# Kernel tuning notes

Hardware: AMD Instinct MI355X
Metric: run time of the kernel (lower is better)

Reference implementation:

```python
import jax, jax.numpy as jnp
import numpy as np

H = 16  # attention heads


def setup_inputs() -> dict:
    key = jax.random.key(0)
    k0, k1, k2 = jax.random.split(key, 3)
    B, T, C = 2, 2048, 1024
    x = jax.random.normal(k0, (B, T, C), dtype=jnp.float32)
    W_attn = jax.random.normal(k1, (3 * C, C), dtype=jnp.float32) * 0.02
    W_proj = jax.random.normal(k2, (C, C), dtype=jnp.float32) * 0.02
    b_proj = jnp.zeros((C,), dtype=jnp.float32)
    return {"x": x, "W_attn": W_attn, "W_proj": W_proj, "b_proj": b_proj}


def reference(x, W_attn, W_proj, b_proj):
    # Eval-mode (dropout = identity), rotational_embeddings=False, flash=False path.
    B, T, C = x.shape
    d = C // H
    qkv = jnp.einsum('btc,fc->btf', x, W_attn)          # [B,T,3C] fused QKV proj
    q, k, v = jnp.split(qkv, 3, axis=-1)
    # [B,T,C] -> [B,H,T,d]
    q = q.reshape(B, T, H, d).transpose(0, 2, 1, 3)
    k = k.reshape(B, T, H, d).transpose(0, 2, 1, 3)
    v = v.reshape(B, T, H, d).transpose(0, 2, 1, 3)
    scale = 1.0 / np.sqrt(d).astype(np.float32)
    att = jnp.einsum('bhqd,bhkd->bhqk', q, k) * scale    # full TxT scores (no mask)
    att = jax.nn.softmax(att, axis=-1)
    y = jnp.einsum('bhqk,bhkd->bhqd', att, v)            # [B,H,T,d]
    y = y.transpose(0, 2, 1, 3).reshape(B, T, C)
    return jnp.einsum('btc,oc->bto', y, W_proj) + b_proj
```

## Files before the change

### kernel.cpp

```cpp
#include <hip/hip_runtime.h>
#include <hip/hip_bf16.h>
#include <stdint.h>

typedef __attribute__((ext_vector_type(8))) short bf16x8;
typedef __attribute__((ext_vector_type(4))) float f32x4;
typedef __attribute__((ext_vector_type(4))) unsigned u32x4;

#define MFMA16(A,B,C) __builtin_amdgcn_mfma_f32_16x16x32_bf16(A,B,C,0,0,0)


__device__ inline void gld_lds16(const __hip_bfloat16* g, __hip_bfloat16* l) {
  __builtin_amdgcn_global_load_lds(
      (const __attribute__((address_space(1))) void*)g,
      (__attribute__((address_space(3))) void*)l, 16, 0, 0);
}

__device__ inline unsigned pkbf(float a, float b) {
  __hip_bfloat162 t = __float22bfloat162_rn(float2{a, b});
  return *(unsigned*)&t;
}

__device__ inline void quad_mix(unsigned &a, unsigned &b) {
#if __has_builtin(__builtin_amdgcn_permlane32_swap) && __has_builtin(__builtin_amdgcn_permlane16_swap)
  auto r1 = __builtin_amdgcn_permlane32_swap(a, b, false, false);
  auto r2 = __builtin_amdgcn_permlane16_swap(r1[0], r1[1], false, false);
  a = r2[0];
  b = r2[1];
#else
  int lane = (int)(threadIdx.x & 63);
  int g = lane >> 4;
  int lm = lane & 15;
  int slo = (((g << 1) & 3) << 4) | lm;
  int shi = ((((g << 1) | 1) & 3) << 4) | lm;
  unsigned t0 = (unsigned)__shfl((int)a, slo, 64);
  unsigned t1 = (unsigned)__shfl((int)b, slo, 64);
  unsigned t2 = (unsigned)__shfl((int)a, shi, 64);
  unsigned t3 = (unsigned)__shfl((int)b, shi, 64);
  bool hi = g >= 2;
  unsigned na = hi ? t1 : t0;
  unsigned nb = hi ? t3 : t2;
  a = na;
  b = nb;
#endif
}

__global__ __launch_bounds__(256)
void cvt_bf16(const float* __restrict__ s0, __hip_bfloat16* __restrict__ d0, int n0,
              const float* __restrict__ s1, __hip_bfloat16* __restrict__ d1, int n1,
              const float* __restrict__ s2, __hip_bfloat16* __restrict__ d2, int n2)
{
  const float* s; __hip_bfloat16* d; int n;
  if      (blockIdx.y == 0) { s = s0; d = d0; n = n0; }
  else if (blockIdx.y == 1) { s = s1; d = d1; n = n1; }
  else                      { s = s2; d = d2; n = n2; }
  int idx = (blockIdx.x * 256 + threadIdx.x) * 8;
  if (idx >= n) return;
  float4 u0 = *(const float4*)(s + idx);
  float4 u1 = *(const float4*)(s + idx + 4);
  __hip_bfloat16 t[8];
  t[0] = __float2bfloat16(u0.x); t[1] = __float2bfloat16(u0.y);
  t[2] = __float2bfloat16(u0.z); t[3] = __float2bfloat16(u0.w);
  t[4] = __float2bfloat16(u1.x); t[5] = __float2bfloat16(u1.y);
  t[6] = __float2bfloat16(u1.z); t[7] = __float2bfloat16(u1.w);
  *(int4*)(d + idx) = *(const int4*)t;
}

template<int BM, int BN, typename TC>
__global__ __launch_bounds__(256)
void gemm_bt(const __hip_bfloat16* __restrict__ A,
             const __hip_bfloat16* __restrict__ B,
             TC* __restrict__ C,
             const float* __restrict__ bias,
             __hip_bfloat16* __restrict__ vtg,
             int M, int N, int K)
{
  constexpr int MI = BM / 32;
  constexpr int NJ = BN / 32;
  constexpr int NP = (BM + BN) / 64;

  __shared__ __align__(16) __hip_bfloat16 As[BM * 32];
  __shared__ __align__(16) __hip_bfloat16 Bs[BN * 32];

  const int tid  = threadIdx.x;
  const int lane = tid & 63;
  const int w    = tid >> 6;
  const int lm   = lane & 15;
  const int g    = lane >> 4;

  const int bm = blockIdx.y * BM;
  const int bn = blockIdx.x * BN;
  const int rm = (w >> 1) * (BM / 2);
  const int cn = (w & 1) * (BN / 2);

  const f32x4 fzero = {0.0f, 0.0f, 0.0f, 0.0f};
  f32x4 acc[MI][NJ];
  for (int i = 0; i < MI; i++)
    for (int j = 0; j < NJ; j++)
      acc[i][j] = fzero;

  for (int k0 = 0; k0 < K; k0 += 32) {
    __syncthreads();
#pragma unroll
    for (int p = 0; p < NP; p++) {
      int c = tid + p * 256;
      if (c < BM * 4)
        gld_lds16(&A[(size_t)(bm + (c >> 2)) * K + k0 + (c & 3) * 8], &As[c * 8]);
      else {
        int cb = c - BM * 4;
        gld_lds16(&B[(size_t)(bn + (cb >> 2)) * K + k0 + (cb & 3) * 8], &Bs[cb * 8]);
      }
    }
    __syncthreads();

    bf16x8 af[MI], bfr[NJ];
#pragma unroll
    for (int i = 0; i < MI; i++)
      af[i] = *(const bf16x8*)&As[(rm + 16 * i + lm) * 32 + 8 * g];
#pragma unroll
    for (int j = 0; j < NJ; j++)
      bfr[j] = *(const bf16x8*)&Bs[(cn + 16 * j + lm) * 32 + 8 * g];
#pragma unroll
    for (int i = 0; i < MI; i++)
#pragma unroll
      for (int j = 0; j < NJ; j++)
        acc[i][j] = MFMA16(af[i], bfr[j], acc[i][j]);
  }

  if (vtg != nullptr && bn >= 2048) {
#pragma unroll
    for (int j = 0; j < NJ; j++) {
      int colv = bn + cn + 16 * j + lm - 2048;
      int vh = colv >> 6, dd = colv & 63;
#pragma unroll
      for (int i = 0; i < MI; i++) {
        int m0 = bm + rm + 16 * i + 4 * g;
        int bb = m0 >> 11, t0 = m0 & 2047;
        __hip_bfloat16 t4[4];
#pragma unroll
        for (int r = 0; r < 4; r++) t4[r] = __float2bfloat16(acc[i][j][r]);
        *(int2*)&vtg[((size_t)(bb * 16 + vh) * 64 + dd) * 2048 + t0] =
            *(const int2*)t4;
      }
    }
    return;
  }

  const float qs = (vtg != nullptr && bn < 1024) ? (0.125f * 1.4426950408889634f)
                                                 : 1.0f;
#pragma unroll
  for (int j = 0; j < NJ; j++) {
    int coln = bn + cn + 16 * j + lm;
    float bv = bias ? bias[coln] : 0.0f;
#pragma unroll
    for (int i = 0; i < MI; i++) {
#pragma unroll
      for (int r = 0; r < 4; r++) {
        int rowm = bm + rm + 16 * i + 4 * g + r;
        float v = acc[i][j][r] * qs + bv;
        if constexpr (sizeof(TC) == 2)
          C[(size_t)rowm * N + coln] = __float2bfloat16(v);
        else
          C[(size_t)rowm * N + coln] = v;
      }
    }
  }
}

__global__ __launch_bounds__(256)
void mha(const __hip_bfloat16* __restrict__ qkv,
         const __hip_bfloat16* __restrict__ vtg,
         __hip_bfloat16* __restrict__ yout,
         __hip_bfloat16* __restrict__ po,
         float* __restrict__ pl,
         int nsteps)
{
  const int T = 2048, F = 3072, Cc = 1024;
  const int bh = blockIdx.x;
  const int b  = bh >> 4, h = bh & 15;
  const int qb0 = blockIdx.y * 128;
  const int z   = blockIdx.z;
  const int kvb = z * 32 * nsteps;

  const int tid  = threadIdx.x;
  const int lane = tid & 63;
  const int w    = tid >> 6;
  const int lm   = lane & 15;
  const int g    = lane >> 4;

  __shared__ __align__(16) __hip_bfloat16 Ks[2][32 * 64];
  __shared__ __align__(16) __hip_bfloat16 Vs[2][64 * 32];

  const size_t rowbase = (size_t)b * T * F;
  const int hoff = h * 64;
  const __hip_bfloat16* Kbase = qkv + rowbase + 1024 + hoff;
  const __hip_bfloat16* Vtb   = vtg + (size_t)(b * 16 + h) * 64 * 2048;

  const int qw = qb0 + 32 * w;
  bf16x8 aq[2][2];
#pragma unroll
  for (int mt = 0; mt < 2; mt++)
#pragma unroll
    for (int e = 0; e < 2; e++)
      aq[mt][e] = *(const bf16x8*)
          &qkv[rowbase + (size_t)(qw + 16 * mt + lm) * F + hoff + 32 * e + 8 * g];

  const f32x4 fzero = {0.0f, 0.0f, 0.0f, 0.0f};
  f32x4 yacc[2][4];
  float lsum[2] = {0.0f, 0.0f};
#pragma unroll
  for (int mt = 0; mt < 2; mt++)
#pragma unroll
    for (int c = 0; c < 4; c++) yacc[mt][c] = fzero;

  const int r0  = tid >> 3;
  const int swK = (tid & 7) ^ (r0 & 7);
  const int vdd = tid >> 2;
  const int vk  = (tid & 3) ^ ((tid >> 3) & 3);
  const int sxK = lm & 7;
  const int sxV = (lm >> 1) & 3;

  gld_lds16(Kbase + (size_t)(kvb + r0) * F + swK * 8, &Ks[0][tid * 8]);
  gld_lds16(Vtb + (size_t)vdd * 2048 + kvb + vk * 8, &Vs[0][tid * 8]);

  for (int t = 0; t < nsteps; t++) {
    const int buf = t & 1;
    __syncthreads();
    if (t + 1 < nsteps) {
      const int kvn = kvb + (t + 1) * 32;
      gld_lds16(Kbase + (size_t)(kvn + r0) * F + swK * 8, &Ks[buf ^ 1][tid * 8]);
      gld_lds16(Vtb + (size_t)vdd * 2048 + kvn + vk * 8, &Vs[buf ^ 1][tid * 8]);
    }

    bf16x8 kf[2][2];
#pragma unroll
    for (int c2 = 0; c2 < 2; c2++) {
      kf[c2][0] = *(const bf16x8*)&Ks[buf][(16 * c2 + lm) * 64 + ((0 + g) ^ sxK) * 8];
      kf[c2][1] = *(const bf16x8*)&Ks[buf][(16 * c2 + lm) * 64 + ((4 + g) ^ sxK) * 8];
    }
#pragma unroll
    for (int mt = 0; mt < 2; mt++) {
      f32x4 st[2];
#pragma unroll
      for (int c2 = 0; c2 < 2; c2++) {
        st[c2] = MFMA16(kf[c2][0], aq[mt][0], fzero);
        st[c2] = MFMA16(kf[c2][1], aq[mt][1], st[c2]);
      }

      unsigned pkv[2][2];
#pragma unroll
      for (int c2 = 0; c2 < 2; c2++)
#pragma unroll
        for (int u = 0; u < 2; u++) {
          float p0 = __builtin_amdgcn_exp2f(st[c2][2 * u]);
          float p1 = __builtin_amdgcn_exp2f(st[c2][2 * u + 1]);
          lsum[mt] += p0 + p1;
          pkv[c2][u] = pkbf(p0, p1);
        }

      unsigned f0 = pkv[0][0], f2 = pkv[1][0];
      quad_mix(f0, f2);
      unsigned f1 = pkv[0][1], f3 = pkv[1][1];
      quad_mix(f1, f3);
      u32x4 fv = {f0, f1, f2, f3};
      bf16x8 ap = __builtin_bit_cast(bf16x8, fv);

#pragma unroll
      for (int c = 0; c < 4; c++) {
        bf16x8 bv = *(const bf16x8*)&Vs[buf][(16 * c + lm) * 32 + (g ^ sxV) * 8];
        yacc[mt][c] = MFMA16(ap, bv, yacc[mt][c]);
      }
    }
  }

  float lred[2];
#pragma unroll
  for (int mt = 0; mt < 2; mt++) {
    float ls = lsum[mt];
    ls += __shfl_xor(ls, 16);
    ls += __shfl_xor(ls, 32);
    lred[mt] = ls;
  }

#pragma unroll
  for (int mt = 0; mt < 2; mt++) {
    if (yout != nullptr) {
      float rv[4];
#pragma unroll
      for (int r = 0; r < 4; r++)
        rv[r] = 1.0f / __shfl(lred[mt], 4 * g + r, 64);
#pragma unroll
      for (int c = 0; c < 4; c++)
#pragma unroll
        for (int r = 0; r < 4; r++) {
          int qrow = qw + 16 * mt + 4 * g + r;
          yout[(size_t)(b * T + qrow) * Cc + hoff + 16 * c + lm] =
              __float2bfloat16(yacc[mt][c][r] * rv[r]);
        }
    } else {
      __hip_bfloat16* pz = po + (size_t)z * 4096 * 1024;
      float* plz = pl + (size_t)z * 4096 * 16;
#pragma unroll
      for (int c = 0; c < 4; c++)
#pragma unroll
        for (int r = 0; r < 4; r++) {
          int qrow = qw + 16 * mt + 4 * g + r;
          pz[(size_t)(b * T + qrow) * Cc + hoff + 16 * c + lm] =
              __float2bfloat16(yacc[mt][c][r]);
        }
      if (lane < 16)
        plz[(b * T + qw + 16 * mt + lane) * 16 + h] = lred[mt];
    }
  }
}

__global__ __launch_bounds__(256)
void combine(const __hip_bfloat16* __restrict__ po,
             const float* __restrict__ pl,
             __hip_bfloat16* __restrict__ y)
{
  int idx = (blockIdx.x * 256 + threadIdx.x) * 8;
  int row = idx >> 10, c = idx & 1023, h = c >> 6;
  float la = pl[row * 16 + h];
  float lb = pl[4096 * 16 + row * 16 + h];
  float rinv = 1.0f / (la + lb);
  const __hip_bfloat16* pa = po + idx;
  const __hip_bfloat16* pb = po + 4096 * 1024 + idx;
  __hip_bfloat16 t[8];
#pragma unroll
  for (int j = 0; j < 8; j++)
    t[j] = __float2bfloat16(
        (__bfloat162float(pa[j]) + __bfloat162float(pb[j])) * rinv);
  *(int4*)(y + idx) = *(const int4*)t;
}

extern "C" void kernel_launch(void* const* d_in, const int* in_sizes, int n_in,
                              void* d_out, int out_size, void* d_ws, size_t ws_size,
                              hipStream_t stream)
{
  const float* x  = (const float*)d_in[0];
  const float* Wa = (const float*)d_in[1];
  const float* Wp = (const float*)d_in[2];
  const float* bp = (const float*)d_in[3];
  float* out = (float*)d_out;

  const int BT = 4096, C = 1024, F3 = 3072;
  char* ws = (char*)d_ws;
  __hip_bfloat16* qkv  = (__hip_bfloat16*)ws;
  __hip_bfloat16* vtg  = (__hip_bfloat16*)(ws + 25165824);
  __hip_bfloat16* xbf  = (__hip_bfloat16*)(ws + 33554432);
  __hip_bfloat16* yb   = xbf;
  __hip_bfloat16* Wabf = (__hip_bfloat16*)(ws + 41943040);
  __hip_bfloat16* Wpbf = (__hip_bfloat16*)(ws + 48234496);
  __hip_bfloat16* Opar = (__hip_bfloat16*)(ws + 50331648);
  float*          lpar = (float*)(ws + 67108864);
  const size_t need_split = 67633152;

  cvt_bf16<<<dim3(2048, 3), 256, 0, stream>>>(
      x, xbf, BT * C, Wa, Wabf, F3 * C, Wp, Wpbf, C * C);
  gemm_bt<128, 128, __hip_bfloat16>
      <<<dim3(F3 / 128, BT / 128), 256, 0, stream>>>(xbf, Wabf, qkv, nullptr, vtg,
                                                     BT, F3, C);
  if (ws_size >= need_split) {
    mha<<<dim3(32, 16, 2), 256, 0, stream>>>(qkv, vtg, nullptr, Opar, lpar, 32);
    combine<<<dim3(BT * C / 2048), 256, 0, stream>>>(Opar, lpar, yb);
  } else {
    mha<<<dim3(32, 16, 1), 256, 0, stream>>>(qkv, vtg, yb, nullptr, nullptr, 64);
  }
  gemm_bt<64, 128, float>
      <<<dim3(C / 128, BT / 64), 256, 0, stream>>>(yb, Wpbf, out, bp, nullptr,
                                                   BT, C, C);
}
```

Before: 206.6 us.

## Fuse fp32-to-bf16 conversion and split-KV combine into GEMM tile loads

Removes the separate conversion kernel and the combine kernel. The QKV GEMM now reads fp32 x and W_attn directly and converts them to bf16 while staging into LDS. The output GEMM merges the two split-KV partials and normalizes them while loading its A tile, and its tile grows to 128x128. This saves two launches and the bf16 intermediate round trips to memory, but the GEMM loads become synchronous register loads instead of async global-to-LDS copies, and the weights are reconverted by every block that reads them. The non-split fallback path is also dropped.

```diff
diff --git a/kernel.cpp b/kernel.cpp
--- a/kernel.cpp
+++ b/kernel.cpp
@@ -13,6 +13,37 @@
   __builtin_amdgcn_global_load_lds(
       (const __attribute__((address_space(1))) void*)g,
       (__attribute__((address_space(3))) void*)l, 16, 0, 0);
+}
+
+__device__ inline void cvt_store8(const float* __restrict__ g,
+                                  __hip_bfloat16* __restrict__ l) {
+  float4 u0 = *(const float4*)g;
+  float4 u1 = *(const float4*)(g + 4);
+  __hip_bfloat162 t[4];
+  t[0] = __float22bfloat162_rn(float2{u0.x, u0.y});
+  t[1] = __float22bfloat162_rn(float2{u0.z, u0.w});
+  t[2] = __float22bfloat162_rn(float2{u1.x, u1.y});
+  t[3] = __float22bfloat162_rn(float2{u1.z, u1.w});
+  *(int4*)l = *(const int4*)t;
+}
+
+__device__ inline void comb_store8(const __hip_bfloat16* __restrict__ a,
+                                   const __hip_bfloat16* __restrict__ b,
+                                   float rinv,
+                                   __hip_bfloat16* __restrict__ l) {
+  int4 av = *(const int4*)a;
+  int4 bv = *(const int4*)b;
+  const __hip_bfloat162* ap = (const __hip_bfloat162*)&av;
+  const __hip_bfloat162* bp = (const __hip_bfloat162*)&bv;
+  __hip_bfloat162 t[4];
+#pragma unroll
+  for (int i = 0; i < 4; i++) {
+    float2 fa = __bfloat1622float2(ap[i]);
+    float2 fb = __bfloat1622float2(bp[i]);
+    t[i] = __float22bfloat162_rn(float2{(fa.x + fb.x) * rinv,
+                                        (fa.y + fb.y) * rinv});
+  }
+  *(int4*)l = *(const int4*)t;
 }
 
 __device__ inline unsigned pkbf(float a, float b) {
@@ -45,41 +76,14 @@
 }
 
 __global__ __launch_bounds__(256)
-void cvt_bf16(const float* __restrict__ s0, __hip_bfloat16* __restrict__ d0, int n0,
-              const float* __restrict__ s1, __hip_bfloat16* __restrict__ d1, int n1,
-              const float* __restrict__ s2, __hip_bfloat16* __restrict__ d2, int n2)
+void gemm_qkv(const float* __restrict__ A,
+              const float* __restrict__ B,
+              __hip_bfloat16* __restrict__ C,
+              __hip_bfloat16* __restrict__ vtg,
+              int M, int N, int K)
 {
-  const float* s; __hip_bfloat16* d; int n;
-  if      (blockIdx.y == 0) { s = s0; d = d0; n = n0; }
-  else if (blockIdx.y == 1) { s = s1; d = d1; n = n1; }
-  else                      { s = s2; d = d2; n = n2; }
-  int idx = (blockIdx.x * 256 + threadIdx.x) * 8;
-  if (idx >= n) return;
-  float4 u0 = *(const float4*)(s + idx);
-  float4 u1 = *(const float4*)(s + idx + 4);
-  __hip_bfloat16 t[8];
-  t[0] = __float2bfloat16(u0.x); t[1] = __float2bfloat16(u0.y);
-  t[2] = __float2bfloat16(u0.z); t[3] = __float2bfloat16(u0.w);
-  t[4] = __float2bfloat16(u1.x); t[5] = __float2bfloat16(u1.y);
-  t[6] = __float2bfloat16(u1.z); t[7] = __float2bfloat16(u1.w);
-  *(int4*)(d + idx) = *(const int4*)t;
-}
-
-template<int BM, int BN, typename TC>
-__global__ __launch_bounds__(256)
-void gemm_bt(const __hip_bfloat16* __restrict__ A,
-             const __hip_bfloat16* __restrict__ B,
-             TC* __restrict__ C,
-             const float* __restrict__ bias,
-             __hip_bfloat16* __restrict__ vtg,
-             int M, int N, int K)
-{
-  constexpr int MI = BM / 32;
-  constexpr int NJ = BN / 32;
-  constexpr int NP = (BM + BN) / 64;
-
-  __shared__ __align__(16) __hip_bfloat16 As[BM * 32];
-  __shared__ __align__(16) __hip_bfloat16 Bs[BN * 32];
+  __shared__ __align__(16) __hip_bfloat16 As[128 * 32];
+  __shared__ __align__(16) __hip_bfloat16 Bs[128 * 32];
 
   const int tid  = threadIdx.x;
   const int lane = tid & 63;
@@ -87,52 +91,51 @@
   const int lm   = lane & 15;
   const int g    = lane >> 4;
 
-  const int bm = blockIdx.y * BM;
-  const int bn = blockIdx.x * BN;
-  const int rm = (w >> 1) * (BM / 2);
-  const int cn = (w & 1) * (BN / 2);
+  const int bm = blockIdx.y * 128;
+  const int bn = blockIdx.x * 128;
+  const int rm = (w >> 1) * 64;
+  const int cn = (w & 1) * 64;
+
+  const int row0 = tid >> 2;
+  const int kc   = (tid & 3) * 8;
 
   const f32x4 fzero = {0.0f, 0.0f, 0.0f, 0.0f};
-  f32x4 acc[MI][NJ];
-  for (int i = 0; i < MI; i++)
-    for (int j = 0; j < NJ; j++)
+  f32x4 acc[4][4];
+  for (int i = 0; i < 4; i++)
+    for (int j = 0; j < 4; j++)
       acc[i][j] = fzero;
 
   for (int k0 = 0; k0 < K; k0 += 32) {
     __syncthreads();
 #pragma unroll
-    for (int p = 0; p < NP; p++) {
-      int c = tid + p * 256;
-      if (c < BM * 4)
-        gld_lds16(&A[(size_t)(bm + (c >> 2)) * K + k0 + (c & 3) * 8], &As[c * 8]);
-      else {
-        int cb = c - BM * 4;
-        gld_lds16(&B[(size_t)(bn + (cb >> 2)) * K + k0 + (cb & 3) * 8], &Bs[cb * 8]);
-      }
-    }
-    __syncthreads();
-
-    bf16x8 af[MI], bfr[NJ];
-#pragma unroll
-    for (int i = 0; i < MI; i++)
+    for (int p = 0; p < 2; p++) {
+      int row = row0 + 64 * p;
+      cvt_store8(A + (size_t)(bm + row) * K + k0 + kc, &As[row * 32 + kc]);
+      cvt_store8(B + (size_t)(bn + row) * K + k0 + kc, &Bs[row * 32 + kc]);
+    }
+    __syncthreads();
+
+    bf16x8 af[4], bfr[4];
+#pragma unroll
+    for (int i = 0; i < 4; i++)
       af[i] = *(const bf16x8*)&As[(rm + 16 * i + lm) * 32 + 8 * g];
 #pragma unroll
-    for (int j = 0; j < NJ; j++)
+    for (int j = 0; j < 4; j++)
       bfr[j] = *(const bf16x8*)&Bs[(cn + 16 * j + lm) * 32 + 8 * g];
 #pragma unroll
-    for (int i = 0; i < MI; i++)
-#pragma unroll
-      for (int j = 0; j < NJ; j++)
+    for (int i = 0; i < 4; i++)
+#pragma unroll
+      for (int j = 0; j < 4; j++)
         acc[i][j] = MFMA16(af[i], bfr[j], acc[i][j]);
   }
 
-  if (vtg != nullptr && bn >= 2048) {
-#pragma unroll
-    for (int j = 0; j < NJ; j++) {
+  if (bn >= 2048) {
+#pragma unroll
+    for (int j = 0; j < 4; j++) {
       int colv = bn + cn + 16 * j + lm - 2048;
       int vh = colv >> 6, dd = colv & 63;
 #pragma unroll
-      for (int i = 0; i < MI; i++) {
+      for (int i = 0; i < 4; i++) {
         int m0 = bm + rm + 16 * i + 4 * g;
         int bb = m0 >> 11, t0 = m0 & 2047;
         __hip_bfloat16 t4[4];
@@ -145,22 +148,93 @@
     return;
   }
 
-  const float qs = (vtg != nullptr && bn < 1024) ? (0.125f * 1.4426950408889634f)
-                                                 : 1.0f;
-#pragma unroll
-  for (int j = 0; j < NJ; j++) {
+  const float qs = (bn < 1024) ? (0.125f * 1.4426950408889634f) : 1.0f;
+#pragma unroll
+  for (int j = 0; j < 4; j++) {
     int coln = bn + cn + 16 * j + lm;
-    float bv = bias ? bias[coln] : 0.0f;
-#pragma unroll
-    for (int i = 0; i < MI; i++) {
+#pragma unroll
+    for (int i = 0; i < 4; i++) {
 #pragma unroll
       for (int r = 0; r < 4; r++) {
         int rowm = bm + rm + 16 * i + 4 * g + r;
-        float v = acc[i][j][r] * qs + bv;
-        if constexpr (sizeof(TC) == 2)
-          C[(size_t)rowm * N + coln] = __float2bfloat16(v);
-        else
-          C[(size_t)rowm * N + coln] = v;
+        C[(size_t)rowm * N + coln] = __float2bfloat16(acc[i][j][r] * qs);
+      }
+    }
+  }
+}
+
+__global__ __launch_bounds__(256)
+void gemm_out(const __hip_bfloat16* __restrict__ po,
+              const float* __restrict__ pl,
+              const float* __restrict__ Bw,
+              const float* __restrict__ bias,
+              float* __restrict__ out,
+              int M, int N, int K)
+{
+  __shared__ __align__(16) __hip_bfloat16 As[128 * 32];
+  __shared__ __align__(16) __hip_bfloat16 Bs[128 * 32];
+
+  const int tid  = threadIdx.x;
+  const int lane = tid & 63;
+  const int w    = tid >> 6;
+  const int lm   = lane & 15;
+  const int g    = lane >> 4;
+
+  const int bm = blockIdx.y * 128;
+  const int bn = blockIdx.x * 128;
+  const int rm = (w >> 1) * 64;
+  const int cn = (w & 1) * 64;
+
+  const int row0 = tid >> 2;
+  const int kc   = (tid & 3) * 8;
+
+  const f32x4 fzero = {0.0f, 0.0f, 0.0f, 0.0f};
+  f32x4 acc[4][4];
+  for (int i = 0; i < 4; i++)
+    for (int j = 0; j < 4; j++)
+      acc[i][j] = fzero;
+
+  for (int k0 = 0; k0 < K; k0 += 32) {
+    const int h = (k0 + kc) >> 6;
+    __syncthreads();
+#pragma unroll
+    for (int p = 0; p < 2; p++) {
+      int row = row0 + 64 * p;
+      int m = bm + row;
+      float la = pl[m * 16 + h];
+      float lb = pl[4096 * 16 + m * 16 + h];
+      float rinv = 1.0f / (la + lb);
+      comb_store8(po + (size_t)m * 1024 + k0 + kc,
+                  po + (size_t)4096 * 1024 + (size_t)m * 1024 + k0 + kc,
+                  rinv, &As[row * 32 + kc]);
+      cvt_store8(Bw + (size_t)(bn + row) * K + k0 + kc, &Bs[row * 32 + kc]);
+    }
+    __syncthreads();
+
+    bf16x8 af[4], bfr[4];
+#pragma unroll
+    for (int i = 0; i < 4; i++)
+      af[i] = *(const bf16x8*)&As[(rm + 16 * i + lm) * 32 + 8 * g];
+#pragma unroll
+    for (int j = 0; j < 4; j++)
+      bfr[j] = *(const bf16x8*)&Bs[(cn + 16 * j + lm) * 32 + 8 * g];
+#pragma unroll
+    for (int i = 0; i < 4; i++)
+#pragma unroll
+      for (int j = 0; j < 4; j++)
+        acc[i][j] = MFMA16(af[i], bfr[j], acc[i][j]);
+  }
+
+#pragma unroll
+  for (int j = 0; j < 4; j++) {
+    int coln = bn + cn + 16 * j + lm;
+    float bv = bias[coln];
+#pragma unroll
+    for (int i = 0; i < 4; i++) {
+#pragma unroll
+      for (int r = 0; r < 4; r++) {
+        int rowm = bm + rm + 16 * i + 4 * g + r;
+        out[(size_t)rowm * N + coln] = acc[i][j][r] + bv;
       }
     }
   }
@@ -169,7 +243,6 @@
 __global__ __launch_bounds__(256)
 void mha(const __hip_bfloat16* __restrict__ qkv,
          const __hip_bfloat16* __restrict__ vtg,
-         __hip_bfloat16* __restrict__ yout,
          __hip_bfloat16* __restrict__ po,
          float* __restrict__ pl,
          int nsteps)
@@ -281,56 +354,21 @@
     lred[mt] = ls;
   }
 
+  __hip_bfloat16* pz = po + (size_t)z * 4096 * 1024;
+  float* plz = pl + (size_t)z * 4096 * 16;
 #pragma unroll
   for (int mt = 0; mt < 2; mt++) {
-    if (yout != nullptr) {
-      float rv[4];
-#pragma unroll
-      for (int r = 0; r < 4; r++)
-        rv[r] = 1.0f / __shfl(lred[mt], 4 * g + r, 64);
-#pragma unroll
-      for (int c = 0; c < 4; c++)
-#pragma unroll
-        for (int r = 0; r < 4; r++) {
-          int qrow = qw + 16 * mt + 4 * g + r;
-          yout[(size_t)(b * T + qrow) * Cc + hoff + 16 * c + lm] =
-              __float2bfloat16(yacc[mt][c][r] * rv[r]);
-        }
-    } else {
-      __hip_bfloat16* pz = po + (size_t)z * 4096 * 1024;
-      float* plz = pl + (size_t)z * 4096 * 16;
-#pragma unroll
-      for (int c = 0; c < 4; c++)
-#pragma unroll
-        for (int r = 0; r < 4; r++) {
-          int qrow = qw + 16 * mt + 4 * g + r;
-          pz[(size_t)(b * T + qrow) * Cc + hoff + 16 * c + lm] =
-              __float2bfloat16(yacc[mt][c][r]);
-        }
-      if (lane < 16)
-        plz[(b * T + qw + 16 * mt + lane) * 16 + h] = lred[mt];
-    }
-  }
-}
-
-__global__ __launch_bounds__(256)
-void combine(const __hip_bfloat16* __restrict__ po,
-             const float* __restrict__ pl,
-             __hip_bfloat16* __restrict__ y)
-{
-  int idx = (blockIdx.x * 256 + threadIdx.x) * 8;
-  int row = idx >> 10, c = idx & 1023, h = c >> 6;
-  float la = pl[row * 16 + h];
-  float lb = pl[4096 * 16 + row * 16 + h];
-  float rinv = 1.0f / (la + lb);
-  const __hip_bfloat16* pa = po + idx;
-  const __hip_bfloat16* pb = po + 4096 * 1024 + idx;
-  __hip_bfloat16 t[8];
-#pragma unroll
-  for (int j = 0; j < 8; j++)
-    t[j] = __float2bfloat16(
-        (__bfloat162float(pa[j]) + __bfloat162float(pb[j])) * rinv);
-  *(int4*)(y + idx) = *(const int4*)t;
+#pragma unroll
+    for (int c = 0; c < 4; c++)
+#pragma unroll
+      for (int r = 0; r < 4; r++) {
+        int qrow = qw + 16 * mt + 4 * g + r;
+        pz[(size_t)(b * T + qrow) * Cc + hoff + 16 * c + lm] =
+            __float2bfloat16(yacc[mt][c][r]);
+      }
+    if (lane < 16)
+      plz[(b * T + qw + 16 * mt + lane) * 16 + h] = lred[mt];
+  }
 }
 
 extern "C" void kernel_launch(void* const* d_in, const int* in_sizes, int n_in,
@@ -347,26 +385,12 @@
   char* ws = (char*)d_ws;
   __hip_bfloat16* qkv  = (__hip_bfloat16*)ws;
   __hip_bfloat16* vtg  = (__hip_bfloat16*)(ws + 25165824);
-  __hip_bfloat16* xbf  = (__hip_bfloat16*)(ws + 33554432);
-  __hip_bfloat16* yb   = xbf;
-  __hip_bfloat16* Wabf = (__hip_bfloat16*)(ws + 41943040);
-  __hip_bfloat16* Wpbf = (__hip_bfloat16*)(ws + 48234496);
-  __hip_bfloat16* Opar = (__hip_bfloat16*)(ws + 50331648);
-  float*          lpar = (float*)(ws + 67108864);
-  const size_t need_split = 67633152;
-
-  cvt_bf16<<<dim3(2048, 3), 256, 0, stream>>>(
-      x, xbf, BT * C, Wa, Wabf, F3 * C, Wp, Wpbf, C * C);
-  gemm_bt<128, 128, __hip_bfloat16>
-      <<<dim3(F3 / 128, BT / 128), 256, 0, stream>>>(xbf, Wabf, qkv, nullptr, vtg,
-                                                     BT, F3, C);
-  if (ws_size >= need_split) {
-    mha<<<dim3(32, 16, 2), 256, 0, stream>>>(qkv, vtg, nullptr, Opar, lpar, 32);
-    combine<<<dim3(BT * C / 2048), 256, 0, stream>>>(Opar, lpar, yb);
-  } else {
-    mha<<<dim3(32, 16, 1), 256, 0, stream>>>(qkv, vtg, yb, nullptr, nullptr, 64);
-  }
-  gemm_bt<64, 128, float>
-      <<<dim3(C / 128, BT / 64), 256, 0, stream>>>(yb, Wpbf, out, bp, nullptr,
-                                                   BT, C, C);
-}
+  __hip_bfloat16* Opar = (__hip_bfloat16*)(ws + 33554432);
+  float*          lpar = (float*)(ws + 50331648);
+
+  gemm_qkv<<<dim3(F3 / 128, BT / 128), 256, 0, stream>>>(x, Wa, qkv, vtg,
+                                                         BT, F3, C);
+  mha<<<dim3(32, 16, 2), 256, 0, stream>>>(qkv, vtg, Opar, lpar, 32);
+  gemm_out<<<dim3(C / 128, BT / 128), 256, 0, stream>>>(Opar, lpar, Wp, bp, out,
+                                                        BT, C, C);
+}
```

Measured after the change: 223.5 us. 1.08x slower.
